# Kernel tuning notes

Hardware: AMD Instinct MI355X
Metric: run time of the kernel (lower is better)

The kernel has to match this reference:

```python
import jax, jax.numpy as jnp
import numpy as np

D_MODEL, NHEAD, DIM_FF = 256, 8, 2048
B, Q, HW = 8, 100, 128 * 128
EPS = 1e-5


def _layernorm(x, g, b):
    mu = jnp.mean(x, axis=-1, keepdims=True)
    var = jnp.mean(jnp.square(x - mu), axis=-1, keepdims=True)
    return (x - mu) * jax.lax.rsqrt(var + EPS) * g + b


def _mha(x_q, x_kv, in_w, in_b, out_w, out_b, nhead, mask=None):
    """torch.nn.MultiheadAttention (batch_first). mask: (B*H,Q,S) bool, True=ATTEND."""
    d = x_q.shape[-1]
    wq, wk, wv = jnp.split(in_w, 3, axis=0)
    bq, bk, bv = jnp.split(in_b, 3)
    q = x_q @ wq.T + bq          # (B,Q,d)
    k = x_kv @ wk.T + bk         # (B,S,d)
    v = x_kv @ wv.T + bv
    Bb, Qq, _ = q.shape
    S = k.shape[1]
    hd = d // nhead
    q = q.reshape(Bb, Qq, nhead, hd).transpose(0, 2, 1, 3)   # (B,H,Q,hd)
    k = k.reshape(Bb, S, nhead, hd).transpose(0, 2, 1, 3)    # (B,H,S,hd)
    v = v.reshape(Bb, S, nhead, hd).transpose(0, 2, 1, 3)
    scores = jnp.einsum('bhqd,bhkd->bhqk', q, k) / jnp.sqrt(jnp.asarray(hd, q.dtype))
    if mask is not None:
        m = mask.reshape(Bb, nhead, Qq, S)
        scores = jnp.where(m, scores, -jnp.inf)
    attn = jax.nn.softmax(scores, axis=-1)
    out = jnp.einsum('bhqk,bhkd->bhqd', attn, v)             # (B,H,Q,hd)
    out = out.transpose(0, 2, 1, 3).reshape(Bb, Qq, d)
    return out @ out_w.T + out_b


def setup_inputs() -> dict:
    key = jax.random.key(0)
    ks = jax.random.split(key, 10)
    s = 0.02
    return {
        'queries': jax.random.normal(ks[0], (B, Q, D_MODEL), jnp.float32),
        'pixel_features': jax.random.normal(ks[1], (B, HW, D_MODEL), jnp.float32),
        'attn_mask': jax.random.randint(ks[2], (B * NHEAD, Q, HW), 0, 2).astype(bool),
        'sa_in_w': jax.random.normal(ks[3], (3 * D_MODEL, D_MODEL), jnp.float32) * s,
        'sa_in_b': jnp.zeros((3 * D_MODEL,), jnp.float32),
        'sa_out_w': jax.random.normal(ks[4], (D_MODEL, D_MODEL), jnp.float32) * s,
        'sa_out_b': jnp.zeros((D_MODEL,), jnp.float32),
        'norm1_g': jnp.ones((D_MODEL,), jnp.float32),
        'norm1_b': jnp.zeros((D_MODEL,), jnp.float32),
        'ca_in_w': jax.random.normal(ks[5], (3 * D_MODEL, D_MODEL), jnp.float32) * s,
        'ca_in_b': jnp.zeros((3 * D_MODEL,), jnp.float32),
        'ca_out_w': jax.random.normal(ks[6], (D_MODEL, D_MODEL), jnp.float32) * s,
        'ca_out_b': jnp.zeros((D_MODEL,), jnp.float32),
        'norm2_g': jnp.ones((D_MODEL,), jnp.float32),
        'norm2_b': jnp.zeros((D_MODEL,), jnp.float32),
        'ff_w1': jax.random.normal(ks[7], (DIM_FF, D_MODEL), jnp.float32) * s,
        'ff_b1': jnp.zeros((DIM_FF,), jnp.float32),
        'ff_w2': jax.random.normal(ks[8], (D_MODEL, DIM_FF), jnp.float32) * s,
        'ff_b2': jnp.zeros((D_MODEL,), jnp.float32),
        'norm3_g': jnp.ones((D_MODEL,), jnp.float32),
        'norm3_b': jnp.zeros((D_MODEL,), jnp.float32),
    }


def reference(queries, pixel_features, attn_mask,
              sa_in_w, sa_in_b, sa_out_w, sa_out_b, norm1_g, norm1_b,
              ca_in_w, ca_in_b, ca_out_w, ca_out_b, norm2_g, norm2_b,
              ff_w1, ff_b1, ff_w2, ff_b2, norm3_g, norm3_b):
    # 1) self-attention among queries (post-norm residual)
    sa = _mha(queries, queries, sa_in_w, sa_in_b, sa_out_w, sa_out_b, NHEAD)
    x = _layernorm(queries + sa, norm1_g, norm1_b)
    # 2) masked cross-attention (attn_mask: True = attend)
    ca = _mha(x, pixel_features, ca_in_w, ca_in_b, ca_out_w, ca_out_b, NHEAD, mask=attn_mask)
    x = _layernorm(x + ca, norm2_g, norm2_b)
    # 3) FFN
    h = jax.nn.relu(x @ ff_w1.T + ff_b1)
    ff = h @ ff_w2.T + ff_b2
    return _layernorm(x + ff, norm3_g, norm3_b)
```

## Files before the change

kernel.cpp:

```cpp
#include <hip/hip_runtime.h>

#define SCALE 0.17677669529663687f
#define SCALE2 (0.17677669529663687f * 1.4426950408889634f)

typedef __attribute__((ext_vector_type(8))) short frag8;
typedef __attribute__((ext_vector_type(4))) float facc4;

#define MFMA16(a, b, c) __builtin_amdgcn_mfma_f32_16x16x32_bf16((a), (b), (c), 0, 0, 0)

__device__ __forceinline__ unsigned short f2b(float f) {
  union { float f; unsigned u; } v; v.f = f;
  return (unsigned short)((v.u + 0x7fffu + ((v.u >> 16) & 1u)) >> 16);
}
__device__ __forceinline__ float b2f(unsigned short h) {
  union { unsigned u; float f; } v; v.u = ((unsigned)h) << 16;
  return v.f;
}
__device__ __forceinline__ unsigned int pack2(float a, float b) {
  return (unsigned int)f2b(a) | ((unsigned int)f2b(b) << 16);
}
__device__ __forceinline__ unsigned int tpack(float a, float b) {
  union { float f; unsigned u; } x, y; x.f = a; y.f = b;
  return (x.u >> 16) | (y.u & 0xffff0000u);
}
__device__ __forceinline__ void gl_lds16(const void* g, void* l) {
  __builtin_amdgcn_global_load_lds((const __attribute__((address_space(1))) unsigned int*)g,
                                   (__attribute__((address_space(3))) unsigned int*)l, 16, 0, 0);
}

union F8U { frag8 f; unsigned u[4]; };

__global__ __launch_bounds__(256) void cvt_weights(const float* __restrict__ s0, const float* __restrict__ s1,
                                                   const float* __restrict__ s2, const float* __restrict__ s3,
                                                   const float* __restrict__ s4, const float* __restrict__ s5,
                                                   unsigned short* __restrict__ dst) {
  int bid = blockIdx.x;
  const float* src; int off;
  if (bid < 96)       { src = s0; off = 0; }
  else if (bid < 128) { src = s1; off = 196608; bid -= 96; }
  else if (bid < 224) { src = s2; off = 262144; bid -= 128; }
  else if (bid < 256) { src = s3; off = 458752; bid -= 224; }
  else if (bid < 512) { src = s4; off = 524288; bid -= 256; }
  else                { src = s5; off = 1048576; bid -= 512; }
  int i = bid * 2048 + threadIdx.x * 8;
  float4 a = *(const float4*)(src + i);
  float4 b = *(const float4*)(src + i + 4);
  uint4 p;
  p.x = pack2(a.x, a.y); p.y = pack2(a.z, a.w);
  p.z = pack2(b.x, b.y); p.w = pack2(b.z, b.w);
  *(uint4*)(dst + off + i) = p;
}

template <int RELU, int BIAS>
__global__ __launch_bounds__(256) void mfma_gemm(const float* __restrict__ A,
                                                 const unsigned short* __restrict__ Wb,
                                                 const float* __restrict__ bias,
                                                 float* __restrict__ C,
                                                 int M, int N, int Ktot, int Kchunk) {
  __shared__ unsigned short As[64 * 40];
  __shared__ unsigned short Bs[64 * 32];
  const int t = threadIdx.x;
  const int mb = blockIdx.x, nb = blockIdx.y, zb = blockIdx.z;
  const int w = t >> 6, lane = t & 63, quad = lane >> 4, l16 = lane & 15;
  const int kbeg = zb * Kchunk;
  float* Cz = C + (size_t)zb * M * N;
  facc4 acc[4] = {};
  for (int k0 = kbeg; k0 < kbeg + Kchunk; k0 += 32) {
    {
      int r = t >> 2, c = (t & 3) * 8;
      int gr = mb * 64 + r;
      float4 f0 = {}, f1 = {};
      if (gr < M) {
        const float* src = A + (size_t)gr * Ktot + k0 + c;
        f0 = *(const float4*)src; f1 = *(const float4*)(src + 4);
      }
      uint4 p;
      p.x = pack2(f0.x, f0.y); p.y = pack2(f0.z, f0.w);
      p.z = pack2(f1.x, f1.y); p.w = pack2(f1.z, f1.w);
      *(uint4*)&As[r * 40 + c] = p;
    }
    {
      int row = w * 16 + (lane >> 2);
      gl_lds16(Wb + (size_t)(nb * 64 + row) * Ktot + k0 + (lane & 3) * 8, Bs + w * 512);
    }
    __syncthreads();
    frag8 af = *(const frag8*)(As + (w * 16 + l16) * 40 + quad * 8);
#pragma unroll
    for (int nt = 0; nt < 4; ++nt) {
      frag8 bf = *(const frag8*)(Bs + (nt * 16 + l16) * 32 + quad * 8);
      acc[nt] = MFMA16(af, bf, acc[nt]);
    }
    __syncthreads();
  }
#pragma unroll
  for (int nt = 0; nt < 4; ++nt)
#pragma unroll
    for (int rg = 0; rg < 4; ++rg) {
      int row = mb * 64 + w * 16 + quad * 4 + rg;
      int col = nb * 64 + nt * 16 + l16;
      if (row < M) {
        float v = acc[nt][rg] + (BIAS ? bias[col] : 0.f);
        if (RELU) v = fmaxf(v, 0.f);
        Cz[(size_t)row * N + col] = v;
      }
    }
}

__global__ __launch_bounds__(256) void res_ln(const float* __restrict__ y,
                                              const float* __restrict__ resid,
                                              const float* __restrict__ g,
                                              const float* __restrict__ bv,
                                              float* __restrict__ out) {
  const int r = blockIdx.x, t = threadIdx.x;
  float v = y[(size_t)r * 256 + t] + resid[(size_t)r * 256 + t];
  __shared__ float red[8];
  float s1 = v, s2 = v * v;
#pragma unroll
  for (int off = 1; off < 64; off <<= 1) { s1 += __shfl_xor(s1, off, 64); s2 += __shfl_xor(s2, off, 64); }
  if ((t & 63) == 0) { red[t >> 6] = s1; red[4 + (t >> 6)] = s2; }
  __syncthreads();
  float S1 = red[0] + red[1] + red[2] + red[3];
  float S2 = red[4] + red[5] + red[6] + red[7];
  float mu = S1 * (1.f / 256.f);
  float var = S2 * (1.f / 256.f) - mu * mu;
  float inv = rsqrtf(var + 1e-5f);
  out[(size_t)r * 256 + t] = (v - mu) * inv * g[t] + bv[t];
}

__global__ __launch_bounds__(256) void res_ln4(const float* __restrict__ p,
                                               const float* __restrict__ bias,
                                               const float* __restrict__ resid,
                                               const float* __restrict__ g,
                                               const float* __restrict__ bv,
                                               float* __restrict__ out) {
  const int r = blockIdx.x, t = threadIdx.x;
  size_t i = (size_t)r * 256 + t;
  float v = p[i] + p[i + 204800] + p[i + 409600] + p[i + 614400] + bias[t] + resid[i];
  __shared__ float red[8];
  float s1 = v, s2 = v * v;
#pragma unroll
  for (int off = 1; off < 64; off <<= 1) { s1 += __shfl_xor(s1, off, 64); s2 += __shfl_xor(s2, off, 64); }
  if ((t & 63) == 0) { red[t >> 6] = s1; red[4 + (t >> 6)] = s2; }
  __syncthreads();
  float S1 = red[0] + red[1] + red[2] + red[3];
  float S2 = red[4] + red[5] + red[6] + red[7];
  float mu = S1 * (1.f / 256.f);
  float var = S2 * (1.f / 256.f) - mu * mu;
  float inv = rsqrtf(var + 1e-5f);
  out[i] = (v - mu) * inv * g[t] + bv[t];
}

__global__ __launch_bounds__(256) void self_attn(const float* __restrict__ qkv,
                                                 float* __restrict__ out) {
  const int wid = blockIdx.x * 4 + (threadIdx.x >> 6);
  const int lane = threadIdx.x & 63;
  const int bh = wid / 100, q = wid - bh * 100;
  const int b = bh >> 3, h = bh & 7;
  float4 qv[8];
  {
    const float4* qr = (const float4*)(qkv + (size_t)(b * 100 + q) * 768 + h * 32);
#pragma unroll
    for (int i = 0; i < 8; ++i) {
      float4 x = qr[i];
      qv[i] = make_float4(x.x * SCALE, x.y * SCALE, x.z * SCALE, x.w * SCALE);
    }
  }
  float l = 0.f;
  float4 O[8] = {};
  for (int k0 = 0; k0 < 128; k0 += 64) {
    int k = k0 + lane;
    int kc = (k < 100) ? k : 0;
    const float4* kr = (const float4*)(qkv + (size_t)(b * 100 + kc) * 768 + 256 + h * 32);
    float s = 0.f;
#pragma unroll
    for (int i = 0; i < 8; ++i) {
      float4 kx = kr[i];
      s += qv[i].x * kx.x + qv[i].y * kx.y + qv[i].z * kx.z + qv[i].w * kx.w;
    }
    float p = (k < 100) ? __expf(s) : 0.f;
    l += p;
    const float4* vr = (const float4*)(qkv + (size_t)(b * 100 + kc) * 768 + 512 + h * 32);
#pragma unroll
    for (int i = 0; i < 8; ++i) {
      float4 vx = vr[i];
      O[i].x += p * vx.x; O[i].y += p * vx.y; O[i].z += p * vx.z; O[i].w += p * vx.w;
    }
  }
#pragma unroll
  for (int off = 1; off < 64; off <<= 1) {
    l += __shfl_xor(l, off, 64);
#pragma unroll
    for (int i = 0; i < 8; ++i) {
      O[i].x += __shfl_xor(O[i].x, off, 64);
      O[i].y += __shfl_xor(O[i].y, off, 64);
      O[i].z += __shfl_xor(O[i].z, off, 64);
      O[i].w += __shfl_xor(O[i].w, off, 64);
    }
  }
  if (lane < 32) {
    float inv = 1.f / l;
    int i4 = lane >> 2, sub = lane & 3;
    float ov = 0.f;
#pragma unroll
    for (int i = 0; i < 8; ++i) {
      if (i4 == i) {
        float4 vv = O[i];
        ov = (sub == 0) ? vv.x : (sub == 1) ? vv.y : (sub == 2) ? vv.z : vv.w;
      }
    }
    out[(size_t)(b * 100 + q) * 256 + h * 32 + lane] = ov * inv;
  }
}

__global__ __launch_bounds__(512, 2) void ca_fused(const float* __restrict__ qc,
                                                   const unsigned short* __restrict__ wkv,
                                                   const float* __restrict__ bkv,
                                                   const float* __restrict__ pix,
                                                   const unsigned char* __restrict__ mask,
                                                   unsigned short* __restrict__ Opartb,
                                                   float* __restrict__ lpart) {
  const int bid = blockIdx.x;
  const int b = bid >> 5, chunk = bid & 31;
  const int t = threadIdx.x;
  const int h = t >> 6, lane = t & 63, quad = lane >> 4, l16 = lane & 15;
  const int bh = b * 8 + h;

  __shared__ unsigned short PixS[8 * 32 * 40];

  frag8 qf[7];
#pragma unroll
  for (int qt = 0; qt < 7; ++qt) {
    int r = qt * 16 + l16;
    float4 f0 = {}, f1 = {};
    if (r < 100) {
      const float* qrow = qc + (size_t)(b * 100 + r) * 256 + h * 32 + quad * 4;
      f0 = *(const float4*)qrow;
      f1 = *(const float4*)(qrow + 16);
    }
    F8U u;
    u.u[0] = pack2(f0.x * SCALE2, f0.y * SCALE2);
    u.u[1] = pack2(f0.z * SCALE2, f0.w * SCALE2);
    u.u[2] = pack2(f1.x * SCALE2, f1.y * SCALE2);
    u.u[3] = pack2(f1.z * SCALE2, f1.w * SCALE2);
    qf[qt] = u.f;
  }

  float bK[2][4], bV[2];
#pragma unroll
  for (int mf = 0; mf < 2; ++mf) {
#pragma unroll
    for (int rg = 0; rg < 4; ++rg) bK[mf][rg] = bkv[h * 32 + mf * 16 + quad * 4 + rg];
    bV[mf] = bkv[256 + h * 32 + mf * 16 + l16];
  }

  const unsigned short* wkbase = wkv + (size_t)(h * 32) * 256;
  const unsigned short* wvbase = wkv + (size_t)(256 + h * 32) * 256;

  facc4 o[7][2] = {};
  float lacc[7] = {};
  const facc4 zacc = {0.f, 0.f, 0.f, 0.f};

  for (int it = 0; it < 16; ++it) {
    const int kk = it * 32;
    const int gkey = chunk * 512 + kk;
    __syncthreads();
    {
      int row = t >> 4, cg = (t & 15) * 16;
      const float* src = pix + ((size_t)(b * 16384 + gkey + row)) * 256 + cg;
      float4 a0 = *(const float4*)src;
      float4 a1 = *(const float4*)(src + 4);
      float4 a2 = *(const float4*)(src + 8);
      float4 a3 = *(const float4*)(src + 12);
      uint4 u0, u1;
      u0.x = tpack(a0.x, a0.y); u0.y = tpack(a0.z, a0.w);
      u0.z = tpack(a1.x, a1.y); u0.w = tpack(a1.z, a1.w);
      u1.x = tpack(a2.x, a2.y); u1.y = tpack(a2.z, a2.w);
      u1.z = tpack(a3.x, a3.y); u1.w = tpack(a3.z, a3.w);
      unsigned short* d = PixS + (cg >> 5) * 1280 + row * 40 + (cg & 31);
      *(uint4*)d = u0; *(uint4*)(d + 8) = u1;
    }
    __syncthreads();

    facc4 ka[2][2] = {}, va[2][2] = {};
#pragma unroll
    for (int cb = 0; cb < 8; ++cb) {
      frag8 pf0 = *(const frag8*)(PixS + cb * 1280 + l16 * 40 + quad * 8);
      frag8 pf1 = *(const frag8*)(PixS + cb * 1280 + (16 + l16) * 40 + quad * 8);
      int co = cb * 32 + quad * 8;
      frag8 wk0 = *(const frag8*)(wkbase + (size_t)l16 * 256 + co);
      frag8 wk1 = *(const frag8*)(wkbase + (size_t)(16 + l16) * 256 + co);
      frag8 wv0 = *(const frag8*)(wvbase + (size_t)l16 * 256 + co);
      frag8 wv1 = *(const frag8*)(wvbase + (size_t)(16 + l16) * 256 + co);
      ka[0][0] = MFMA16(wk0, pf0, ka[0][0]); ka[0][1] = MFMA16(wk0, pf1, ka[0][1]);
      ka[1][0] = MFMA16(wk1, pf0, ka[1][0]); ka[1][1] = MFMA16(wk1, pf1, ka[1][1]);
      va[0][0] = MFMA16(pf0, wv0, va[0][0]); va[0][1] = MFMA16(pf0, wv1, va[0][1]);
      va[1][0] = MFMA16(pf1, wv0, va[1][0]); va[1][1] = MFMA16(pf1, wv1, va[1][1]);
    }
    frag8 kfA0, kfA1, vfB0, vfB1;
    {
      F8U k0u, k1u, v0u, v1u;
#pragma unroll
      for (int pr = 0; pr < 4; ++pr) {
        int mf = pr >> 1, r0 = (pr & 1) * 2, r1 = r0 + 1;
        k0u.u[pr] = tpack(ka[mf][0][r0] + bK[mf][r0], ka[mf][0][r1] + bK[mf][r1]);
        k1u.u[pr] = tpack(ka[mf][1][r0] + bK[mf][r0], ka[mf][1][r1] + bK[mf][r1]);
        v0u.u[pr] = tpack(va[mf][0][r0] + bV[0], va[mf][0][r1] + bV[0]);
        v1u.u[pr] = tpack(va[mf][1][r0] + bV[1], va[mf][1][r1] + bV[1]);
      }
      kfA0 = k0u.f; kfA1 = k1u.f; vfB0 = v0u.f; vfB1 = v1u.f;
    }

    const unsigned char* mbase = mask + (size_t)bh * 100 * 16384 + gkey + quad * 4;
#pragma unroll
    for (int qt = 0; qt < 7; ++qt) {
      facc4 s0 = MFMA16(kfA0, qf[qt], zacc);
      facc4 s1 = MFMA16(kfA1, qf[qt], zacc);
      int r = qt * 16 + l16;
      int rc = (r < 100) ? r : 99;
      const unsigned char* mrow = mbase + (size_t)rc * 16384;
      unsigned m0 = *(const unsigned*)mrow;
      unsigned m1 = *(const unsigned*)(mrow + 16);
      if (r >= 100) { m0 = 0; m1 = 0; }
      float p[8];
#pragma unroll
      for (int rg = 0; rg < 4; ++rg) {
        float e0 = exp2f(s0[rg]);
        float e1 = exp2f(s1[rg]);
        p[rg] = ((m0 >> (rg * 8)) & 1u) ? e0 : 0.f;
        p[4 + rg] = ((m1 >> (rg * 8)) & 1u) ? e1 : 0.f;
      }
      lacc[qt] += p[0] + p[1] + p[2] + p[3] + p[4] + p[5] + p[6] + p[7];
      F8U pu;
      pu.u[0] = tpack(p[0], p[1]); pu.u[1] = tpack(p[2], p[3]);
      pu.u[2] = tpack(p[4], p[5]); pu.u[3] = tpack(p[6], p[7]);
      o[qt][0] = MFMA16(pu.f, vfB0, o[qt][0]);
      o[qt][1] = MFMA16(pu.f, vfB1, o[qt][1]);
    }
  }

#pragma unroll
  for (int qt = 0; qt < 7; ++qt) {
    lacc[qt] += __shfl_xor(lacc[qt], 16, 64);
    lacc[qt] += __shfl_xor(lacc[qt], 32, 64);
  }
  unsigned short* Op = Opartb + ((size_t)bh * 32 + chunk) * 112 * 32;
  float* lp = lpart + ((size_t)bh * 32 + chunk) * 112;
#pragma unroll
  for (int qt = 0; qt < 7; ++qt) {
#pragma unroll
    for (int rg = 0; rg < 4; ++rg) {
      int row = qt * 16 + quad * 4 + rg;
      Op[row * 32 + l16] = f2b(o[qt][0][rg]);
      Op[row * 32 + 16 + l16] = f2b(o[qt][1][rg]);
    }
    if (lane < 16) lp[qt * 16 + lane] = lacc[qt];
  }
}

__global__ __launch_bounds__(256) void cross_combine(const unsigned short* __restrict__ Opartb,
                                                     const float* __restrict__ lpart,
                                                     float* __restrict__ out) {
  const int bid = blockIdx.x;
  const int bh = bid / 13, qg = bid - bh * 13;
  const int t = threadIdx.x;
  const int q = qg * 8 + (t >> 5), d = t & 31;
  if (q >= 100) return;
  const int b = bh >> 3, h = bh & 7;
  float osum = 0.f, lsum = 0.f;
#pragma unroll 4
  for (int p = 0; p < 32; ++p) {
    osum += b2f(Opartb[(((size_t)bh * 32 + p) * 112 + q) * 32 + d]);
    lsum += lpart[((size_t)bh * 32 + p) * 112 + q];
  }
  out[(size_t)(b * 100 + q) * 256 + h * 32 + d] = osum / lsum;
}

extern "C" void kernel_launch(void* const* d_in, const int* in_sizes, int n_in,
                              void* d_out, int out_size, void* d_ws, size_t ws_size,
                              hipStream_t stream) {
  const float* queries = (const float*)d_in[0];
  const float* pix = (const float*)d_in[1];
  const unsigned char* mask = (const unsigned char*)d_in[2];
  const float* sa_in_w = (const float*)d_in[3];
  const float* sa_in_b = (const float*)d_in[4];
  const float* sa_out_w = (const float*)d_in[5];
  const float* sa_out_b = (const float*)d_in[6];
  const float* n1g = (const float*)d_in[7];
  const float* n1b = (const float*)d_in[8];
  const float* ca_in_w = (const float*)d_in[9];
  const float* ca_in_b = (const float*)d_in[10];
  const float* ca_out_w = (const float*)d_in[11];
  const float* ca_out_b = (const float*)d_in[12];
  const float* n2g = (const float*)d_in[13];
  const float* n2b = (const float*)d_in[14];
  const float* ff_w1 = (const float*)d_in[15];
  const float* ff_b1 = (const float*)d_in[16];
  const float* ff_w2 = (const float*)d_in[17];
  const float* ff_b2 = (const float*)d_in[18];
  const float* n3g = (const float*)d_in[19];
  const float* n3b = (const float*)d_in[20];
  float* out = (float*)d_out;
  char* ws = (char*)d_ws;

  unsigned short* wb   = (unsigned short*)(ws + 134217728);
  float* qkvs   = (float*)(ws + 152043520);
  float* sao    = (float*)(ws + 154501120);
  float* ptmp   = (float*)(ws + 155320320);
  float* x1     = (float*)(ws + 158597120);
  float* qc     = (float*)(ws + 159416320);
  unsigned short* Opartb = (unsigned short*)(ws + 160235520);
  float* lpart  = (float*)(ws + 189595648);
  float* ca_out = (float*)(ws + 190513152);
  float* x2     = (float*)(ws + 191332352);
  float* hffn   = (float*)(ws + 192151552);

  const unsigned short* wb_sain  = wb;
  const unsigned short* wb_saout = wb + 196608;
  const unsigned short* wb_caq   = wb + 262144;
  const unsigned short* wb_cakv  = wb + 327680;
  const unsigned short* wb_caout = wb + 458752;
  const unsigned short* wb_ff1   = wb + 524288;
  const unsigned short* wb_ff2   = wb + 1048576;

  cvt_weights<<<768, 256, 0, stream>>>(sa_in_w, sa_out_w, ca_in_w, ca_out_w, ff_w1, ff_w2, wb);

  mfma_gemm<0, 1><<<dim3(13, 12, 1), 256, 0, stream>>>(queries, wb_sain, sa_in_b, qkvs, 800, 768, 256, 256);
  self_attn<<<1600, 256, 0, stream>>>(qkvs, sao);
  mfma_gemm<0, 1><<<dim3(13, 4, 1), 256, 0, stream>>>(sao, wb_saout, sa_out_b, ptmp, 800, 256, 256, 256);
  res_ln<<<800, 256, 0, stream>>>(ptmp, queries, n1g, n1b, x1);

  mfma_gemm<0, 1><<<dim3(13, 4, 1), 256, 0, stream>>>(x1, wb_caq, ca_in_b, qc, 800, 256, 256, 256);
  ca_fused<<<256, 512, 0, stream>>>(qc, wb_cakv, ca_in_b + 256, pix, mask, Opartb, lpart);
  cross_combine<<<64 * 13, 256, 0, stream>>>(Opartb, lpart, ca_out);
  mfma_gemm<0, 1><<<dim3(13, 4, 1), 256, 0, stream>>>(ca_out, wb_caout, ca_out_b, ptmp, 800, 256, 256, 256);
  res_ln<<<800, 256, 0, stream>>>(ptmp, x1, n2g, n2b, x2);

  mfma_gemm<1, 1><<<dim3(13, 32, 1), 256, 0, stream>>>(x2, wb_ff1, ff_b1, hffn, 800, 2048, 256, 256);
  mfma_gemm<0, 0><<<dim3(13, 4, 4), 256, 0, stream>>>(hffn, wb_ff2, nullptr, ptmp, 800, 256, 2048, 512);
  res_ln4<<<800, 256, 0, stream>>>(ptmp, ff_b2, x2, n3g, n3b, out);
}
```

Before: 807.7 us.

## Fuse attention epilogues with out-proj, layernorm and q-proj; drop weight pre-conversion

Removes the standalone bf16 weight conversion kernel; GEMMs now convert fp32 weights on the fly, and only the cross-attention KV weights get converted, inside the new sa_epi kernel. sa_epi fuses the self-attention out-projection, residual, layernorm1 and the cross-attention Q projection in one 13-block kernel. ca_epi fuses the partial-softmax combine, out-projection, residual and layernorm2 in a 16-block kernel. This cuts several launches and intermediate round trips. The cost is very low parallelism in the fused kernels (13 and 16 blocks), and every block re-reads and converts full fp32 weights.

```diff
diff --git a/kernel.cpp b/kernel.cpp
--- a/kernel.cpp
+++ b/kernel.cpp
@@ -23,37 +23,12 @@
   union { float f; unsigned u; } x, y; x.f = a; y.f = b;
   return (x.u >> 16) | (y.u & 0xffff0000u);
 }
-__device__ __forceinline__ void gl_lds16(const void* g, void* l) {
-  __builtin_amdgcn_global_load_lds((const __attribute__((address_space(1))) unsigned int*)g,
-                                   (__attribute__((address_space(3))) unsigned int*)l, 16, 0, 0);
-}
 
 union F8U { frag8 f; unsigned u[4]; };
-
-__global__ __launch_bounds__(256) void cvt_weights(const float* __restrict__ s0, const float* __restrict__ s1,
-                                                   const float* __restrict__ s2, const float* __restrict__ s3,
-                                                   const float* __restrict__ s4, const float* __restrict__ s5,
-                                                   unsigned short* __restrict__ dst) {
-  int bid = blockIdx.x;
-  const float* src; int off;
-  if (bid < 96)       { src = s0; off = 0; }
-  else if (bid < 128) { src = s1; off = 196608; bid -= 96; }
-  else if (bid < 224) { src = s2; off = 262144; bid -= 128; }
-  else if (bid < 256) { src = s3; off = 458752; bid -= 224; }
-  else if (bid < 512) { src = s4; off = 524288; bid -= 256; }
-  else                { src = s5; off = 1048576; bid -= 512; }
-  int i = bid * 2048 + threadIdx.x * 8;
-  float4 a = *(const float4*)(src + i);
-  float4 b = *(const float4*)(src + i + 4);
-  uint4 p;
-  p.x = pack2(a.x, a.y); p.y = pack2(a.z, a.w);
-  p.z = pack2(b.x, b.y); p.w = pack2(b.z, b.w);
-  *(uint4*)(dst + off + i) = p;
-}
 
 template <int RELU, int BIAS>
 __global__ __launch_bounds__(256) void mfma_gemm(const float* __restrict__ A,
-                                                 const unsigned short* __restrict__ Wb,
+                                                 const float* __restrict__ W,
                                                  const float* __restrict__ bias,
                                                  float* __restrict__ C,
                                                  int M, int N, int Ktot, int Kchunk) {
@@ -80,8 +55,13 @@
       *(uint4*)&As[r * 40 + c] = p;
     }
     {
-      int row = w * 16 + (lane >> 2);
-      gl_lds16(Wb + (size_t)(nb * 64 + row) * Ktot + k0 + (lane & 3) * 8, Bs + w * 512);
+      int r = t >> 2, c = (t & 3) * 8;
+      const float* src = W + (size_t)(nb * 64 + r) * Ktot + k0 + c;
+      float4 f0 = *(const float4*)src, f1 = *(const float4*)(src + 4);
+      uint4 p;
+      p.x = pack2(f0.x, f0.y); p.y = pack2(f0.z, f0.w);
+      p.z = pack2(f1.x, f1.y); p.w = pack2(f1.z, f1.w);
+      *(uint4*)&Bs[r * 32 + c] = p;
     }
     __syncthreads();
     frag8 af = *(const frag8*)(As + (w * 16 + l16) * 40 + quad * 8);
@@ -104,27 +84,6 @@
         Cz[(size_t)row * N + col] = v;
       }
     }
-}
-
-__global__ __launch_bounds__(256) void res_ln(const float* __restrict__ y,
-                                              const float* __restrict__ resid,
-                                              const float* __restrict__ g,
-                                              const float* __restrict__ bv,
-                                              float* __restrict__ out) {
-  const int r = blockIdx.x, t = threadIdx.x;
-  float v = y[(size_t)r * 256 + t] + resid[(size_t)r * 256 + t];
-  __shared__ float red[8];
-  float s1 = v, s2 = v * v;
-#pragma unroll
-  for (int off = 1; off < 64; off <<= 1) { s1 += __shfl_xor(s1, off, 64); s2 += __shfl_xor(s2, off, 64); }
-  if ((t & 63) == 0) { red[t >> 6] = s1; red[4 + (t >> 6)] = s2; }
-  __syncthreads();
-  float S1 = red[0] + red[1] + red[2] + red[3];
-  float S2 = red[4] + red[5] + red[6] + red[7];
-  float mu = S1 * (1.f / 256.f);
-  float var = S2 * (1.f / 256.f) - mu * mu;
-  float inv = rsqrtf(var + 1e-5f);
-  out[(size_t)r * 256 + t] = (v - mu) * inv * g[t] + bv[t];
 }
 
 __global__ __launch_bounds__(256) void res_ln4(const float* __restrict__ p,
@@ -210,6 +169,166 @@
     }
     out[(size_t)(b * 100 + q) * 256 + h * 32 + lane] = ov * inv;
   }
+}
+
+__global__ __launch_bounds__(256) void sa_epi(const float* __restrict__ sao,
+                                              const float* __restrict__ saow,
+                                              const float* __restrict__ saob,
+                                              const float* __restrict__ queries,
+                                              const float* __restrict__ g1,
+                                              const float* __restrict__ b1,
+                                              const float* __restrict__ caqw,
+                                              const float* __restrict__ caqb,
+                                              const float* __restrict__ cakvw,
+                                              unsigned short* __restrict__ wkvb,
+                                              float* __restrict__ x1,
+                                              float* __restrict__ qc) {
+  __shared__ unsigned short As[64 * 40];
+  __shared__ unsigned short Bs[256 * 32];
+  __shared__ unsigned short Cs[64 * 264];
+  __shared__ float redS[64][5];
+  __shared__ float redQ[64][5];
+  __shared__ float muv[64][2];
+  const int t = threadIdx.x;
+  const int w = t >> 6, lane = t & 63, quad = lane >> 4, l16 = lane & 15;
+  const int r0 = blockIdx.x * 64;
+
+  for (int i = (blockIdx.x * 256 + t) * 8; i < 131072; i += 13 * 256 * 8) {
+    float4 a = *(const float4*)(cakvw + i);
+    float4 b = *(const float4*)(cakvw + i + 4);
+    uint4 p;
+    p.x = pack2(a.x, a.y); p.y = pack2(a.z, a.w);
+    p.z = pack2(b.x, b.y); p.w = pack2(b.z, b.w);
+    *(uint4*)(wkvb + i) = p;
+  }
+
+  facc4 acc[4][4] = {};
+  for (int k0 = 0; k0 < 256; k0 += 32) {
+    {
+      int r = t >> 2, c = (t & 3) * 8;
+      int gr = r0 + r;
+      float4 f0 = {}, f1 = {};
+      if (gr < 800) {
+        const float* s = sao + (size_t)gr * 256 + k0 + c;
+        f0 = *(const float4*)s; f1 = *(const float4*)(s + 4);
+      }
+      uint4 p;
+      p.x = pack2(f0.x, f0.y); p.y = pack2(f0.z, f0.w);
+      p.z = pack2(f1.x, f1.y); p.w = pack2(f1.z, f1.w);
+      *(uint4*)&As[r * 40 + c] = p;
+    }
+    {
+      const float* s = saow + (size_t)t * 256 + k0;
+      float4 a0 = *(const float4*)s, a1 = *(const float4*)(s + 4);
+      float4 a2 = *(const float4*)(s + 8), a3 = *(const float4*)(s + 12);
+      float4 a4 = *(const float4*)(s + 16), a5 = *(const float4*)(s + 20);
+      float4 a6 = *(const float4*)(s + 24), a7 = *(const float4*)(s + 28);
+      uint4 p0, p1;
+      p0.x = pack2(a0.x, a0.y); p0.y = pack2(a0.z, a0.w); p0.z = pack2(a1.x, a1.y); p0.w = pack2(a1.z, a1.w);
+      p1.x = pack2(a2.x, a2.y); p1.y = pack2(a2.z, a2.w); p1.z = pack2(a3.x, a3.y); p1.w = pack2(a3.z, a3.w);
+      *(uint4*)&Bs[t * 32] = p0; *(uint4*)&Bs[t * 32 + 8] = p1;
+      p0.x = pack2(a4.x, a4.y); p0.y = pack2(a4.z, a4.w); p0.z = pack2(a5.x, a5.y); p0.w = pack2(a5.z, a5.w);
+      p1.x = pack2(a6.x, a6.y); p1.y = pack2(a6.z, a6.w); p1.z = pack2(a7.x, a7.y); p1.w = pack2(a7.z, a7.w);
+      *(uint4*)&Bs[t * 32 + 16] = p0; *(uint4*)&Bs[t * 32 + 24] = p1;
+    }
+    __syncthreads();
+    frag8 af[4], bf[4];
+#pragma unroll
+    for (int mt = 0; mt < 4; ++mt) af[mt] = *(const frag8*)(As + (mt * 16 + l16) * 40 + quad * 8);
+#pragma unroll
+    for (int nt = 0; nt < 4; ++nt) bf[nt] = *(const frag8*)(Bs + (w * 64 + nt * 16 + l16) * 32 + quad * 8);
+#pragma unroll
+    for (int mt = 0; mt < 4; ++mt)
+#pragma unroll
+      for (int nt = 0; nt < 4; ++nt) acc[mt][nt] = MFMA16(af[mt], bf[nt], acc[mt][nt]);
+    __syncthreads();
+  }
+#pragma unroll
+  for (int mt = 0; mt < 4; ++mt)
+#pragma unroll
+    for (int nt = 0; nt < 4; ++nt) {
+      int col = w * 64 + nt * 16 + l16;
+      float bb = saob[col];
+#pragma unroll
+      for (int rg = 0; rg < 4; ++rg) {
+        int row = mt * 16 + quad * 4 + rg;
+        int gr = r0 + row;
+        float rv = (gr < 800) ? queries[(size_t)gr * 256 + col] : 0.f;
+        Cs[row * 264 + col] = f2b(acc[mt][nt][rg] + bb + rv);
+      }
+    }
+  __syncthreads();
+  {
+    int tr = t >> 2, seg = t & 3;
+    const unsigned short* cr = &Cs[tr * 264 + seg * 64];
+    float s1 = 0.f, s2 = 0.f;
+#pragma unroll 8
+    for (int c = 0; c < 64; ++c) { float v = b2f(cr[c]); s1 += v; s2 += v * v; }
+    redS[tr][seg] = s1; redQ[tr][seg] = s2;
+  }
+  __syncthreads();
+  if (t < 64) {
+    float S1 = redS[t][0] + redS[t][1] + redS[t][2] + redS[t][3];
+    float S2 = redQ[t][0] + redQ[t][1] + redQ[t][2] + redQ[t][3];
+    float mu = S1 * (1.f / 256.f);
+    float var = S2 * (1.f / 256.f) - mu * mu;
+    muv[t][0] = mu; muv[t][1] = rsqrtf(var + 1e-5f);
+  }
+  __syncthreads();
+  {
+    int tr = t >> 2, seg = t & 3;
+    float mu = muv[tr][0], inv = muv[tr][1];
+    int gr = r0 + tr;
+    unsigned short* cr = &Cs[tr * 264 + seg * 64];
+    float* xr = x1 + (size_t)gr * 256 + seg * 64;
+#pragma unroll 8
+    for (int c = 0; c < 64; ++c) {
+      float v = (b2f(cr[c]) - mu) * inv * g1[seg * 64 + c] + b1[seg * 64 + c];
+      cr[c] = f2b(v);
+      if (gr < 800) xr[c] = v;
+    }
+  }
+  __syncthreads();
+  facc4 acc2[4][4] = {};
+  for (int k0 = 0; k0 < 256; k0 += 32) {
+    {
+      const float* s = caqw + (size_t)t * 256 + k0;
+      float4 a0 = *(const float4*)s, a1 = *(const float4*)(s + 4);
+      float4 a2 = *(const float4*)(s + 8), a3 = *(const float4*)(s + 12);
+      float4 a4 = *(const float4*)(s + 16), a5 = *(const float4*)(s + 20);
+      float4 a6 = *(const float4*)(s + 24), a7 = *(const float4*)(s + 28);
+      uint4 p0, p1;
+      p0.x = pack2(a0.x, a0.y); p0.y = pack2(a0.z, a0.w); p0.z = pack2(a1.x, a1.y); p0.w = pack2(a1.z, a1.w);
+      p1.x = pack2(a2.x, a2.y); p1.y = pack2(a2.z, a2.w); p1.z = pack2(a3.x, a3.y); p1.w = pack2(a3.z, a3.w);
+      *(uint4*)&Bs[t * 32] = p0; *(uint4*)&Bs[t * 32 + 8] = p1;
+      p0.x = pack2(a4.x, a4.y); p0.y = pack2(a4.z, a4.w); p0.z = pack2(a5.x, a5.y); p0.w = pack2(a5.z, a5.w);
+      p1.x = pack2(a6.x, a6.y); p1.y = pack2(a6.z, a6.w); p1.z = pack2(a7.x, a7.y); p1.w = pack2(a7.z, a7.w);
+      *(uint4*)&Bs[t * 32 + 16] = p0; *(uint4*)&Bs[t * 32 + 24] = p1;
+    }
+    __syncthreads();
+    frag8 af[4], bf[4];
+#pragma unroll
+    for (int mt = 0; mt < 4; ++mt) af[mt] = *(const frag8*)(Cs + (mt * 16 + l16) * 264 + k0 + quad * 8);
+#pragma unroll
+    for (int nt = 0; nt < 4; ++nt) bf[nt] = *(const frag8*)(Bs + (w * 64 + nt * 16 + l16) * 32 + quad * 8);
+#pragma unroll
+    for (int mt = 0; mt < 4; ++mt)
+#pragma unroll
+      for (int nt = 0; nt < 4; ++nt) acc2[mt][nt] = MFMA16(af[mt], bf[nt], acc2[mt][nt]);
+    __syncthreads();
+  }
+#pragma unroll
+  for (int mt = 0; mt < 4; ++mt)
+#pragma unroll
+    for (int nt = 0; nt < 4; ++nt) {
+      int col = w * 64 + nt * 16 + l16;
+      float bb = caqb[col];
+#pragma unroll
+      for (int rg = 0; rg < 4; ++rg) {
+        int gr = r0 + mt * 16 + quad * 4 + rg;
+        if (gr < 800) qc[(size_t)gr * 256 + col] = acc2[mt][nt][rg] + bb;
+      }
+    }
 }
 
 __global__ __launch_bounds__(512, 2) void ca_fused(const float* __restrict__ qc,
@@ -301,11 +420,11 @@
       F8U k0u, k1u, v0u, v1u;
 #pragma unroll
       for (int pr = 0; pr < 4; ++pr) {
-        int mf = pr >> 1, r0 = (pr & 1) * 2, r1 = r0 + 1;
-        k0u.u[pr] = tpack(ka[mf][0][r0] + bK[mf][r0], ka[mf][0][r1] + bK[mf][r1]);
-        k1u.u[pr] = tpack(ka[mf][1][r0] + bK[mf][r0], ka[mf][1][r1] + bK[mf][r1]);
-        v0u.u[pr] = tpack(va[mf][0][r0] + bV[0], va[mf][0][r1] + bV[0]);
-        v1u.u[pr] = tpack(va[mf][1][r0] + bV[1], va[mf][1][r1] + bV[1]);
+        int mf = pr >> 1, r0v = (pr & 1) * 2, r1v = r0v + 1;
+        k0u.u[pr] = tpack(ka[mf][0][r0v] + bK[mf][r0v], ka[mf][0][r1v] + bK[mf][r1v]);
+        k1u.u[pr] = tpack(ka[mf][1][r0v] + bK[mf][r0v], ka[mf][1][r1v] + bK[mf][r1v]);
+        v0u.u[pr] = tpack(va[mf][0][r0v] + bV[0], va[mf][0][r1v] + bV[0]);
+        v1u.u[pr] = tpack(va[mf][1][r0v] + bV[1], va[mf][1][r1v] + bV[1]);
       }
       kfA0 = k0u.f; kfA1 = k1u.f; vfB0 = v0u.f; vfB1 = v1u.f;
     }
@@ -357,22 +476,128 @@
   }
 }
 
-__global__ __launch_bounds__(256) void cross_combine(const unsigned short* __restrict__ Opartb,
-                                                     const float* __restrict__ lpart,
-                                                     float* __restrict__ out) {
-  const int bid = blockIdx.x;
-  const int bh = bid / 13, qg = bid - bh * 13;
+__global__ __launch_bounds__(256) void ca_epi(const unsigned short* __restrict__ Opartb,
+                                              const float* __restrict__ lpart,
+                                              const float* __restrict__ caow,
+                                              const float* __restrict__ caob,
+                                              const float* __restrict__ x1,
+                                              const float* __restrict__ g2,
+                                              const float* __restrict__ b2v,
+                                              float* __restrict__ x2) {
+  __shared__ unsigned short Ca[64 * 264];
+  __shared__ unsigned short Bs[256 * 32];
+  __shared__ float linv[8][52];
+  __shared__ float redS[64][5];
+  __shared__ float redQ[64][5];
+  __shared__ float muv[64][2];
   const int t = threadIdx.x;
-  const int q = qg * 8 + (t >> 5), d = t & 31;
-  if (q >= 100) return;
-  const int b = bh >> 3, h = bh & 7;
-  float osum = 0.f, lsum = 0.f;
-#pragma unroll 4
-  for (int p = 0; p < 32; ++p) {
-    osum += b2f(Opartb[(((size_t)bh * 32 + p) * 112 + q) * 32 + d]);
-    lsum += lpart[((size_t)bh * 32 + p) * 112 + q];
-  }
-  out[(size_t)(b * 100 + q) * 256 + h * 32 + d] = osum / lsum;
+  const int w = t >> 6, lane = t & 63, quad = lane >> 4, l16 = lane & 15;
+  const int b = blockIdx.x >> 1, half = blockIdx.x & 1;
+  const int q0 = half * 50;
+  const int gr0 = b * 100 + q0;
+
+  for (int i = t; i < 14 * 264; i += 256) Ca[50 * 264 + i] = 0;
+  {
+    int h = w * 2 + (lane >> 5), p = lane & 31;
+    int bh = b * 8 + h;
+    for (int r = 0; r < 50; ++r) {
+      float v = lpart[((size_t)(bh * 32 + p)) * 112 + q0 + r];
+      v += __shfl_xor(v, 1, 64); v += __shfl_xor(v, 2, 64);
+      v += __shfl_xor(v, 4, 64); v += __shfl_xor(v, 8, 64);
+      v += __shfl_xor(v, 16, 64);
+      if (p == 0) linv[h][r] = 1.f / v;
+    }
+  }
+  __syncthreads();
+  {
+    int h = t >> 5, d = t & 31;
+    int bh = b * 8 + h;
+    float accr[25];
+#pragma unroll
+    for (int pass = 0; pass < 2; ++pass) {
+#pragma unroll
+      for (int r = 0; r < 25; ++r) accr[r] = 0.f;
+      for (int p = 0; p < 32; ++p) {
+        const unsigned short* base = Opartb + ((size_t)(bh * 32 + p) * 112 + q0 + pass * 25) * 32 + d;
+#pragma unroll
+        for (int r = 0; r < 25; ++r) accr[r] += b2f(base[r * 32]);
+      }
+#pragma unroll
+      for (int r = 0; r < 25; ++r)
+        Ca[(pass * 25 + r) * 264 + h * 32 + d] = f2b(accr[r] * linv[h][pass * 25 + r]);
+    }
+  }
+  __syncthreads();
+  facc4 acc[4][4] = {};
+  for (int k0 = 0; k0 < 256; k0 += 32) {
+    {
+      const float* s = caow + (size_t)t * 256 + k0;
+      float4 a0 = *(const float4*)s, a1 = *(const float4*)(s + 4);
+      float4 a2 = *(const float4*)(s + 8), a3 = *(const float4*)(s + 12);
+      float4 a4 = *(const float4*)(s + 16), a5 = *(const float4*)(s + 20);
+      float4 a6 = *(const float4*)(s + 24), a7 = *(const float4*)(s + 28);
+      uint4 p0, p1;
+      p0.x = pack2(a0.x, a0.y); p0.y = pack2(a0.z, a0.w); p0.z = pack2(a1.x, a1.y); p0.w = pack2(a1.z, a1.w);
+      p1.x = pack2(a2.x, a2.y); p1.y = pack2(a2.z, a2.w); p1.z = pack2(a3.x, a3.y); p1.w = pack2(a3.z, a3.w);
+      *(uint4*)&Bs[t * 32] = p0; *(uint4*)&Bs[t * 32 + 8] = p1;
+      p0.x = pack2(a4.x, a4.y); p0.y = pack2(a4.z, a4.w); p0.z = pack2(a5.x, a5.y); p0.w = pack2(a5.z, a5.w);
+      p1.x = pack2(a6.x, a6.y); p1.y = pack2(a6.z, a6.w); p1.z = pack2(a7.x, a7.y); p1.w = pack2(a7.z, a7.w);
+      *(uint4*)&Bs[t * 32 + 16] = p0; *(uint4*)&Bs[t * 32 + 24] = p1;
+    }
+    __syncthreads();
+    frag8 af[4], bf[4];
+#pragma unroll
+    for (int mt = 0; mt < 4; ++mt) af[mt] = *(const frag8*)(Ca + (mt * 16 + l16) * 264 + k0 + quad * 8);
+#pragma unroll
+    for (int nt = 0; nt < 4; ++nt) bf[nt] = *(const frag8*)(Bs + (w * 64 + nt * 16 + l16) * 32 + quad * 8);
+#pragma unroll
+    for (int mt = 0; mt < 4; ++mt)
+#pragma unroll
+      for (int nt = 0; nt < 4; ++nt) acc[mt][nt] = MFMA16(af[mt], bf[nt], acc[mt][nt]);
+    __syncthreads();
+  }
+#pragma unroll
+  for (int mt = 0; mt < 4; ++mt)
+#pragma unroll
+    for (int nt = 0; nt < 4; ++nt) {
+      int col = w * 64 + nt * 16 + l16;
+      float bb = caob[col];
+#pragma unroll
+      for (int rg = 0; rg < 4; ++rg) {
+        int row = mt * 16 + quad * 4 + rg;
+        float rv = (row < 50) ? x1[(size_t)(gr0 + row) * 256 + col] : 0.f;
+        Ca[row * 264 + col] = f2b(acc[mt][nt][rg] + bb + rv);
+      }
+    }
+  __syncthreads();
+  {
+    int tr = t >> 2, seg = t & 3;
+    const unsigned short* cr = &Ca[tr * 264 + seg * 64];
+    float s1 = 0.f, s2 = 0.f;
+#pragma unroll 8
+    for (int c = 0; c < 64; ++c) { float v = b2f(cr[c]); s1 += v; s2 += v * v; }
+    redS[tr][seg] = s1; redQ[tr][seg] = s2;
+  }
+  __syncthreads();
+  if (t < 64) {
+    float S1 = redS[t][0] + redS[t][1] + redS[t][2] + redS[t][3];
+    float S2 = redQ[t][0] + redQ[t][1] + redQ[t][2] + redQ[t][3];
+    float mu = S1 * (1.f / 256.f);
+    float var = S2 * (1.f / 256.f) - mu * mu;
+    muv[t][0] = mu; muv[t][1] = rsqrtf(var + 1e-5f);
+  }
+  __syncthreads();
+  {
+    int tr = t >> 2, seg = t & 3;
+    if (tr < 50) {
+      float mu = muv[tr][0], inv = muv[tr][1];
+      const unsigned short* cr = &Ca[tr * 264 + seg * 64];
+      float* xr = x2 + (size_t)(gr0 + tr) * 256 + seg * 64;
+#pragma unroll 8
+      for (int c = 0; c < 64; ++c)
+        xr[c] = (b2f(cr[c]) - mu) * inv * g2[seg * 64 + c] + b2v[seg * 64 + c];
+    }
+  }
 }
 
 extern "C" void kernel_launch(void* const* d_in, const int* in_sizes, int n_in,
@@ -402,40 +627,26 @@
   float* out = (float*)d_out;
   char* ws = (char*)d_ws;
 
-  unsigned short* wb   = (unsigned short*)(ws + 134217728);
-  float* qkvs   = (float*)(ws + 152043520);
-  float* sao    = (float*)(ws + 154501120);
-  float* ptmp   = (float*)(ws + 155320320);
-  float* x1     = (float*)(ws + 158597120);
-  float* qc     = (float*)(ws + 159416320);
-  unsigned short* Opartb = (unsigned short*)(ws + 160235520);
-  float* lpart  = (float*)(ws + 189595648);
-  float* ca_out = (float*)(ws + 190513152);
-  float* x2     = (float*)(ws + 191332352);
-  float* hffn   = (float*)(ws + 192151552);
-
-  const unsigned short* wb_sain  = wb;
-  const unsigned short* wb_saout = wb + 196608;
-  const unsigned short* wb_caq   = wb + 262144;
-  const unsigned short* wb_cakv  = wb + 327680;
-  const unsigned short* wb_caout = wb + 458752;
-  const unsigned short* wb_ff1   = wb + 524288;
-  const unsigned short* wb_ff2   = wb + 1048576;
-
-  cvt_weights<<<768, 256, 0, stream>>>(sa_in_w, sa_out_w, ca_in_w, ca_out_w, ff_w1, ff_w2, wb);
-
-  mfma_gemm<0, 1><<<dim3(13, 12, 1), 256, 0, stream>>>(queries, wb_sain, sa_in_b, qkvs, 800, 768, 256, 256);
+  float* qkvs = (float*)(ws + 0);
+  float* sao  = (float*)(ws + 2457600);
+  float* x1   = (float*)(ws + 3276800);
+  float* qc   = (float*)(ws + 4096000);
+  float* x2   = (float*)(ws + 4915200);
+  float* hffn = (float*)(ws + 5734400);
+  float* ptmp = (float*)(ws + 12288000);
+  unsigned short* wkvb = (unsigned short*)(ws + 15564800);
+  float* lpart = (float*)(ws + 15826944);
+  unsigned short* Opartb = (unsigned short*)(ws + 16744448);
+
+  mfma_gemm<0, 1><<<dim3(13, 12, 1), 256, 0, stream>>>(queries, sa_in_w, sa_in_b, qkvs, 800, 768, 256, 256);
   self_attn<<<1600, 256, 0, stream>>>(qkvs, sao);
-  mfma_gemm<0, 1><<<dim3(13, 4, 1), 256, 0, stream>>>(sao, wb_saout, sa_out_b, ptmp, 800, 256, 256, 256);
-  res_ln<<<800, 256, 0, stream>>>(ptmp, queries, n1g, n1b, x1);
-
-  mfma_gemm<0, 1><<<dim3(13, 4, 1), 256, 0, stream>>>(x1, wb_caq, ca_in_b, qc, 800, 256, 256, 256);
-  ca_fused<<<256, 512, 0, stream>>>(qc, wb_cakv, ca_in_b + 256, pix, mask, Opartb, lpart);
-  cross_combine<<<64 * 13, 256, 0, stream>>>(Opartb, lpart, ca_out);
-  mfma_gemm<0, 1><<<dim3(13, 4, 1), 256, 0, stream>>>(ca_out, wb_caout, ca_out_b, ptmp, 800, 256, 256, 256);
-  res_ln<<<800, 256, 0, stream>>>(ptmp, x1, n2g, n2b, x2);
-
-  mfma_gemm<1, 1><<<dim3(13, 32, 1), 256, 0, stream>>>(x2, wb_ff1, ff_b1, hffn, 800, 2048, 256, 256);
-  mfma_gemm<0, 0><<<dim3(13, 4, 4), 256, 0, stream>>>(hffn, wb_ff2, nullptr, ptmp, 800, 256, 2048, 512);
+  sa_epi<<<13, 256, 0, stream>>>(sao, sa_out_w, sa_out_b, queries, n1g, n1b,
+                                 ca_in_w, ca_in_b, ca_in_w + 65536, wkvb, x1, qc);
+
+  ca_fused<<<256, 512, 0, stream>>>(qc, wkvb, ca_in_b + 256, pix, mask, Opartb, lpart);
+  ca_epi<<<16, 256, 0, stream>>>(Opartb, lpart, ca_out_w, ca_out_b, x1, n2g, n2b, x2);
+
+  mfma_gemm<1, 1><<<dim3(13, 32, 1), 256, 0, stream>>>(x2, ff_w1, ff_b1, hffn, 800, 2048, 256, 256);
+  mfma_gemm<0, 0><<<dim3(13, 4, 4), 256, 0, stream>>>(hffn, ff_w2, nullptr, ptmp, 800, 256, 2048, 512);
   res_ln4<<<800, 256, 0, stream>>>(ptmp, ff_b2, x2, n3g, n3b, out);
 }
```

Measured after the change: 901.1 us. 11.6% more time.

## Double-buffer pixel tiles in LDS with register prefetch in cross-attention kernel

Applied to the files above, without the earlier changes.

The fused cross-attention kernel now keeps two LDS buffers for the pixel tile. Each iteration issues the global loads for the next tile into registers before the K/V projection and attention work, then packs them into the alternate buffer afterwards, with one barrier per iteration instead of two. Launch bounds drop from 2 to 1 blocks per CU. This frees the register budget for the extra prefetch registers but may lower occupancy and with it latency hiding.

```diff
diff --git a/kernel.cpp b/kernel.cpp
--- a/kernel.cpp
+++ b/kernel.cpp
@@ -212,7 +212,7 @@
   }
 }
 
-__global__ __launch_bounds__(512, 2) void ca_fused(const float* __restrict__ qc,
+__global__ __launch_bounds__(512, 1) void ca_fused(const float* __restrict__ qc,
                                                    const unsigned short* __restrict__ wkv,
                                                    const float* __restrict__ bkv,
                                                    const float* __restrict__ pix,
@@ -225,7 +225,11 @@
   const int h = t >> 6, lane = t & 63, quad = lane >> 4, l16 = lane & 15;
   const int bh = b * 8 + h;
 
-  __shared__ unsigned short PixS[8 * 32 * 40];
+  __shared__ unsigned short PixS[2][8 * 32 * 40];
+
+  const int srow = t >> 4, scg = (t & 15) * 16;
+  const float* psrc = pix + ((size_t)(b * 16384 + chunk * 512 + srow)) * 256 + scg;
+  const int sldoff = (scg >> 5) * 1280 + srow * 40 + (scg & 31);
 
   frag8 qf[7];
 #pragma unroll
@@ -260,32 +264,39 @@
   float lacc[7] = {};
   const facc4 zacc = {0.f, 0.f, 0.f, 0.f};
 
+  {
+    float4 a0 = *(const float4*)psrc;
+    float4 a1 = *(const float4*)(psrc + 4);
+    float4 a2 = *(const float4*)(psrc + 8);
+    float4 a3 = *(const float4*)(psrc + 12);
+    uint4 u0, u1;
+    u0.x = tpack(a0.x, a0.y); u0.y = tpack(a0.z, a0.w);
+    u0.z = tpack(a1.x, a1.y); u0.w = tpack(a1.z, a1.w);
+    u1.x = tpack(a2.x, a2.y); u1.y = tpack(a2.z, a2.w);
+    u1.z = tpack(a3.x, a3.y); u1.w = tpack(a3.z, a3.w);
+    unsigned short* d = PixS[0] + sldoff;
+    *(uint4*)d = u0; *(uint4*)(d + 8) = u1;
+  }
+  __syncthreads();
+
   for (int it = 0; it < 16; ++it) {
     const int kk = it * 32;
     const int gkey = chunk * 512 + kk;
-    __syncthreads();
-    {
-      int row = t >> 4, cg = (t & 15) * 16;
-      const float* src = pix + ((size_t)(b * 16384 + gkey + row)) * 256 + cg;
-      float4 a0 = *(const float4*)src;
-      float4 a1 = *(const float4*)(src + 4);
-      float4 a2 = *(const float4*)(src + 8);
-      float4 a3 = *(const float4*)(src + 12);
-      uint4 u0, u1;
-      u0.x = tpack(a0.x, a0.y); u0.y = tpack(a0.z, a0.w);
-      u0.z = tpack(a1.x, a1.y); u0.w = tpack(a1.z, a1.w);
-      u1.x = tpack(a2.x, a2.y); u1.y = tpack(a2.z, a2.w);
-      u1.z = tpack(a3.x, a3.y); u1.w = tpack(a3.z, a3.w);
-      unsigned short* d = PixS + (cg >> 5) * 1280 + row * 40 + (cg & 31);
-      *(uint4*)d = u0; *(uint4*)(d + 8) = u1;
-    }
-    __syncthreads();
+
+    float4 n0, n1, n2, n3;
+    if (it < 15) {
+      const float* s = psrc + (size_t)(it + 1) * 8192;
+      n0 = *(const float4*)s;       n1 = *(const float4*)(s + 4);
+      n2 = *(const float4*)(s + 8); n3 = *(const float4*)(s + 12);
+    }
+
+    const unsigned short* Pb = PixS[it & 1];
 
     facc4 ka[2][2] = {}, va[2][2] = {};
 #pragma unroll
     for (int cb = 0; cb < 8; ++cb) {
-      frag8 pf0 = *(const frag8*)(PixS + cb * 1280 + l16 * 40 + quad * 8);
-      frag8 pf1 = *(const frag8*)(PixS + cb * 1280 + (16 + l16) * 40 + quad * 8);
+      frag8 pf0 = *(const frag8*)(Pb + cb * 1280 + l16 * 40 + quad * 8);
+      frag8 pf1 = *(const frag8*)(Pb + cb * 1280 + (16 + l16) * 40 + quad * 8);
       int co = cb * 32 + quad * 8;
       frag8 wk0 = *(const frag8*)(wkbase + (size_t)l16 * 256 + co);
       frag8 wk1 = *(const frag8*)(wkbase + (size_t)(16 + l16) * 256 + co);
@@ -301,11 +312,11 @@
       F8U k0u, k1u, v0u, v1u;
 #pragma unroll
       for (int pr = 0; pr < 4; ++pr) {
-        int mf = pr >> 1, r0 = (pr & 1) * 2, r1 = r0 + 1;
-        k0u.u[pr] = tpack(ka[mf][0][r0] + bK[mf][r0], ka[mf][0][r1] + bK[mf][r1]);
-        k1u.u[pr] = tpack(ka[mf][1][r0] + bK[mf][r0], ka[mf][1][r1] + bK[mf][r1]);
-        v0u.u[pr] = tpack(va[mf][0][r0] + bV[0], va[mf][0][r1] + bV[0]);
-        v1u.u[pr] = tpack(va[mf][1][r0] + bV[1], va[mf][1][r1] + bV[1]);
+        int mf = pr >> 1, r0v = (pr & 1) * 2, r1v = r0v + 1;
+        k0u.u[pr] = tpack(ka[mf][0][r0v] + bK[mf][r0v], ka[mf][0][r1v] + bK[mf][r1v]);
+        k1u.u[pr] = tpack(ka[mf][1][r0v] + bK[mf][r0v], ka[mf][1][r1v] + bK[mf][r1v]);
+        v0u.u[pr] = tpack(va[mf][0][r0v] + bV[0], va[mf][0][r1v] + bV[0]);
+        v1u.u[pr] = tpack(va[mf][1][r0v] + bV[1], va[mf][1][r1v] + bV[1]);
       }
       kfA0 = k0u.f; kfA1 = k1u.f; vfB0 = v0u.f; vfB1 = v1u.f;
     }
@@ -336,6 +347,17 @@
       o[qt][0] = MFMA16(pu.f, vfB0, o[qt][0]);
       o[qt][1] = MFMA16(pu.f, vfB1, o[qt][1]);
     }
+
+    if (it < 15) {
+      uint4 u0, u1;
+      u0.x = tpack(n0.x, n0.y); u0.y = tpack(n0.z, n0.w);
+      u0.z = tpack(n1.x, n1.y); u0.w = tpack(n1.z, n1.w);
+      u1.x = tpack(n2.x, n2.y); u1.y = tpack(n2.z, n2.w);
+      u1.z = tpack(n3.x, n3.y); u1.w = tpack(n3.z, n3.w);
+      unsigned short* d = PixS[1 - (it & 1)] + sldoff;
+      *(uint4*)d = u0; *(uint4*)(d + 8) = u1;
+    }
+    __syncthreads();
   }
 
 #pragma unroll
```

Measured after the change: 823.6 us. No clear change (+2.0%).
